# Performance work log

Hardware: AMD Instinct MI355X
Metric: run time of the kernel (lower is better)

Reference implementation:

```python
import jax, jax.numpy as jnp
import numpy as np

B, N, J, P = 64, 2048, 32, 64   # instances, ops per instance, jobs, ops per job (N = J*P)
D, H = 128, 128                 # out_size_ope, hidden_size_ope
NEG_SLOPE = 0.2


def _kaiming(key, fan_in, fan_out):
    return jax.random.normal(key, (fan_in, fan_out), jnp.float32) * np.sqrt(2.0 / fan_in)


def _mlp(x, W1, b1, W2, b2):
    # nn.Sequential(Linear, ELU, Linear)
    return jax.nn.elu(x @ W1 + b1) @ W2 + b2


def setup_inputs() -> dict:
    key = jax.random.key(0)
    ks = jax.random.split(key, 4)
    features = jax.random.normal(ks[0], (B, N, D), jnp.float32)
    job_starts = jnp.arange(J, dtype=jnp.int32) * P                      # first op of each job block
    offsets = jax.random.randint(ks[1], (B, J), 0, P)                    # current position within block
    ope_step_batch = job_starts[None, :] + offsets                       # [B, J], step_j in [start_j, end_j]
    end_ope_biases_batch = jnp.broadcast_to(job_starts + (P - 1), (B, J))
    opes_appertain_batch = jnp.broadcast_to(jnp.repeat(jnp.arange(J, dtype=jnp.int32), P)[None, :], (B, N))
    batch_idxes = jnp.arange(B, dtype=jnp.int32)
    inp = {
        'features': features,
        'discount_r': jnp.float32(0.9),
        'ope_step_batch': ope_step_batch,
        'end_ope_biases_batch': end_ope_biases_batch,
        'opes_appertain_batch': opes_appertain_batch,
        'batch_idxes': batch_idxes,
    }
    for i, nm in enumerate(['fw', 'zj', 'pr']):
        k1, k2 = jax.random.split(jax.random.fold_in(ks[2], i))
        inp[nm + '_W1'] = _kaiming(k1, D, H)
        inp[nm + '_b1'] = jnp.zeros((H,), jnp.float32)
        inp[nm + '_W2'] = _kaiming(k2, H, D)
        inp[nm + '_b2'] = jnp.zeros((D,), jnp.float32)
    return inp


def reference(features, discount_r,
              fw_W1, fw_b1, fw_W2, fw_b2,
              zj_W1, zj_b1, zj_W2, zj_b2,
              pr_W1, pr_b1, pr_W2, pr_b2,
              ope_step_batch, end_ope_biases_batch, opes_appertain_batch, batch_idxes):
    # opes_appertain_batch is accepted but unused, exactly like the torch forward.
    f32 = features.dtype
    steps = ope_step_batch[batch_idxes]        # [B, J]
    ends = end_ope_biases_batch[batch_idxes]   # [B, J]
    i = jnp.arange(N)

    # --- per-job descending update loop, vectorized ---
    # op i is updated iff step_j < i <= end_j for its job j; descending order in the
    # original means feat[i-1] is still the ORIGINAL value, so updates are independent.
    memb = (i[None, None, :] > steps[:, :, None]) & (i[None, None, :] <= ends[:, :, None])  # [B,J,N]
    updated = jnp.any(memb, axis=1)                                                         # [B,N]
    step_of = jnp.sum(jnp.where(memb, steps[:, :, None], 0), axis=1)                        # [B,N]
    rpow = discount_r ** (i[None, :] - step_of).astype(f32)                                 # r^(i - step)
    feat_prev = jnp.concatenate([jnp.zeros_like(features[:, :1]), features[:, :-1]], axis=1)
    # aggregate(MEAN): agg_f_w(feat_pre) + agg_f_w(feat_sub * r)
    cand = _mlp(features, fw_W1, fw_b1, fw_W2, fw_b2) + \
           _mlp(feat_prev * rpow[..., None], fw_W1, fw_b1, fw_W2, fw_b2)
    feat1 = jnp.where(updated[..., None], cand, features)

    # --- collect feat at each valid job's current step (step positions are never updated) ---
    collected = jax.vmap(lambda f, s: f[s])(features, steps)   # [B, J, D]
    valid = steps <= ends                                      # [B, J]
    n = jnp.sum(valid, axis=1).astype(f32)                     # [B]
    S = jnp.sum(jnp.where(valid[..., None], collected, 0.0), axis=1)  # [B, D]
    # aggregate_dif: new[j] = agg_z_j((old[j] + r * sum_{k!=j} old[k]) / n)
    mixed = (collected + discount_r * (S[:, None, :] - collected)) / n[:, None, None]
    z = _mlp(mixed, zj_W1, zj_b1, zj_W2, zj_b2)                # [B, J, D]

    # faithful replication of feat_opt[b][save_index[k]] = features_all[k]
    # (writes at op positions equal to JOB indices 0..J-1, for valid jobs)
    head = jnp.where(valid[..., None], z, feat1[:, :J, :])
    feat2 = feat1.at[:, :J, :].set(head)

    out = jax.nn.leaky_relu(_mlp(feat2, pr_W1, pr_b1, pr_W2, pr_b2), NEG_SLOPE)
    return out
```

## Files before the change

### kernel.cpp

```cpp
#include <hip/hip_runtime.h>

#define B_ 64
#define N_ 2048
#define J_ 32
#define D_ 128
#define NEG_SLOPE_ 0.2f

typedef __attribute__((ext_vector_type(4))) float f32x4;
typedef __attribute__((ext_vector_type(8))) __bf16 bf16x8;
typedef __attribute__((ext_vector_type(4))) __bf16 bf16x4;

#define ACT_NONE 0
#define ACT_ELU 1
#define ACT_LEAKY 2

template<int ACT>
__device__ __forceinline__ float apply_act(float v) {
    if constexpr (ACT == ACT_ELU)        return v > 0.f ? v : __expf(v) - 1.f;
    else if constexpr (ACT == ACT_LEAKY) return v >= 0.f ? v : NEG_SLOPE_ * v;
    else return v;
}

__device__ __forceinline__ bf16x8 frag_ld(const __bf16* src, int row, int kc) {
    return *(const bf16x8*)&src[row * D_ + ((kc ^ (row & 7)) << 3)];
}

__device__ __forceinline__ void load_wregs2(const __bf16* __restrict__ wmat,
                                            int wst, int ln, int lq, bf16x8 wr_[4][2]) {
#pragma unroll
    for (int ks = 0; ks < 4; ++ks)
#pragma unroll
        for (int mt = 0; mt < 2; ++mt)
            wr_[ks][mt] = frag_ld(wmat, wst * 32 + mt * 16 + ln, ks * 4 + lq);
}

__device__ __forceinline__ void gemmS(const __bf16* xb, const bf16x8 wr_[4][2],
                                      int ln, int lq, f32x4 acc[2][4]) {
    const f32x4 z = {0.f, 0.f, 0.f, 0.f};
#pragma unroll
    for (int mt = 0; mt < 2; ++mt)
#pragma unroll
        for (int nt = 0; nt < 4; ++nt) acc[mt][nt] = z;
#pragma unroll
    for (int ks = 0; ks < 4; ++ks) {
        const int kc = ks * 4 + lq;
        bf16x8 b[4];
#pragma unroll
        for (int nt = 0; nt < 4; ++nt) b[nt] = frag_ld(xb, nt * 16 + ln, kc);
#pragma unroll
        for (int mt = 0; mt < 2; ++mt)
#pragma unroll
            for (int nt = 0; nt < 4; ++nt)
                acc[mt][nt] = __builtin_amdgcn_mfma_f32_16x16x32_bf16(wr_[ks][mt], b[nt], acc[mt][nt], 0, 0, 0);
    }
}

template<bool INIT>
__device__ __forceinline__ void gemmS32(const __bf16* xb, const bf16x8 wr_[4][2],
                                        int ln, int lq, f32x4 acc[2][2]) {
    if constexpr (INIT) {
        const f32x4 z = {0.f, 0.f, 0.f, 0.f};
        acc[0][0] = z; acc[0][1] = z; acc[1][0] = z; acc[1][1] = z;
    }
#pragma unroll
    for (int ks = 0; ks < 4; ++ks) {
        const int kc = ks * 4 + lq;
        const bf16x8 b0 = frag_ld(xb, ln, kc);
        const bf16x8 b1 = frag_ld(xb, 16 + ln, kc);
#pragma unroll
        for (int mt = 0; mt < 2; ++mt) {
            acc[mt][0] = __builtin_amdgcn_mfma_f32_16x16x32_bf16(wr_[ks][mt], b0, acc[mt][0], 0, 0, 0);
            acc[mt][1] = __builtin_amdgcn_mfma_f32_16x16x32_bf16(wr_[ks][mt], b1, acc[mt][1], 0, 0, 0);
        }
    }
}

template<int ACT>
__device__ __forceinline__ void epiS_lds(const f32x4 acc[2][4], __bf16* dst,
                                         const float* __restrict__ bias,
                                         int wst, int ln, int lq) {
#pragma unroll
    for (int mt = 0; mt < 2; ++mt) {
        const int cb = wst * 32 + mt * 16 + lq * 4;
        const f32x4 bv = *(const f32x4*)&bias[cb];
#pragma unroll
        for (int nt = 0; nt < 4; ++nt) {
            const int jr = nt * 16 + ln;
            bf16x4 o;
#pragma unroll
            for (int r = 0; r < 4; ++r)
                o[r] = (__bf16)apply_act<ACT>(acc[mt][nt][r] + bv[r]);
            *(bf16x4*)&dst[jr * D_ + (((cb >> 3) ^ (jr & 7)) << 3) + (cb & 7)] = o;
        }
    }
}

template<int ACT>
__device__ __forceinline__ void epiS32_lds(const f32x4 acc[2][2], __bf16* dst, int rowoff,
                                           const float* __restrict__ bias,
                                           int wst, int ln, int lq) {
#pragma unroll
    for (int mt = 0; mt < 2; ++mt) {
        const int cb = wst * 32 + mt * 16 + lq * 4;
        const f32x4 bv = *(const f32x4*)&bias[cb];
#pragma unroll
        for (int nt = 0; nt < 2; ++nt) {
            const int jr = rowoff + nt * 16 + ln;
            bf16x4 o;
#pragma unroll
            for (int r = 0; r < 4; ++r)
                o[r] = (__bf16)apply_act<ACT>(acc[mt][nt][r] + bv[r]);
            *(bf16x4*)&dst[jr * D_ + (((cb >> 3) ^ (jr & 7)) << 3) + (cb & 7)] = o;
        }
    }
}

__global__ __launch_bounds__(256) void k_prep(
    const float* __restrict__ w0, const float* __restrict__ w1,
    const float* __restrict__ w2, const float* __restrict__ w3,
    const float* __restrict__ w4, const float* __restrict__ w5,
    __bf16* __restrict__ wdst,
    const float* __restrict__ F, const int* __restrict__ STEP,
    const int* __restrict__ ENDB, const int* __restrict__ BIDX,
    float* __restrict__ Sbuf, int* __restrict__ nvalid) {
    const int t = threadIdx.x;
    if (blockIdx.x < 6) {
        const float* src;
        switch (blockIdx.x) {
            case 0: src = w0; break; case 1: src = w1; break; case 2: src = w2; break;
            case 3: src = w3; break; case 4: src = w4; break; default: src = w5; break;
        }
        __bf16* d = wdst + (size_t)blockIdx.x * D_ * D_;
        for (int id = t; id < D_ * 16; id += 256) {
            const int n = id >> 4, ch = id & 15;
            bf16x8 u;
#pragma unroll
            for (int j = 0; j < 8; ++j) u[j] = (__bf16)src[(ch * 8 + j) * D_ + n];
            *(bf16x8*)&d[n * D_ + ((ch ^ (n & 7)) << 3)] = u;
        }
        return;
    }
    const int b = blockIdx.x - 6;
    __shared__ int steps_s[J_];
    __shared__ int valid_s[J_];
    __shared__ int nv;
    const int bi = BIDX[b];
    if (t == 0) nv = 0;
    __syncthreads();
    if (t < J_) {
        const int s = STEP[bi * J_ + t];
        const int e = ENDB[bi * J_ + t];
        steps_s[t] = s;
        const int v = (s <= e) ? 1 : 0;
        valid_s[t] = v;
        if (v) atomicAdd(&nv, 1);
    }
    __syncthreads();
    if (t < D_) {
        float acc = 0.f;
        for (int j = 0; j < J_; ++j)
            if (valid_s[j]) acc += F[((size_t)b * N_ + steps_s[j]) * D_ + t];
        Sbuf[b * D_ + t] = acc;
    }
    if (t == 0) nvalid[b] = nv;
}

__global__ __launch_bounds__(256, 4) void k_fused(
    const float* __restrict__ F, const float* __restrict__ rp_,
    const __bf16* __restrict__ wsW,
    const float* __restrict__ fb1, const float* __restrict__ fb2,
    const float* __restrict__ zb1, const float* __restrict__ zb2,
    const float* __restrict__ pb1, const float* __restrict__ pb2,
    const int* __restrict__ STEP, const int* __restrict__ ENDB,
    const int* __restrict__ BIDX, const float* __restrict__ Sbuf,
    const int* __restrict__ nvalid, float* __restrict__ out) {
    __shared__ __bf16 xs[64 * D_];
    __shared__ __bf16 hs[64 * D_];

    const int t = threadIdx.x;
    const int lane = t & 63, wst = t >> 6;
    const int ln = lane & 15, lq = lane >> 4;
    const int bid = blockIdx.x;
    const int b = bid >> 6, ti = bid & 63;
    const int r0 = ti * 32;
    const int bi = BIDX[b];
    const int jb = ti >> 1;
    const int s_j = STEP[bi * J_ + jb];
    const int e_j = ENDB[bi * J_ + jb];
    const float r = *rp_;
    const float l2r = __log2f(r);
    const int lo = (s_j + 1 > r0) ? s_j + 1 : r0;
    const int hi = (e_j < r0 + 31) ? e_j : r0 + 31;
    const bool has_upd = lo <= hi;
    const bool head_tile = (ti == 0);

    const float* Fb = F + (size_t)b * N_ * D_;
    const int nstage = (has_upd ? 64 : 32) * 16;
    for (int id = t; id < nstage; id += 256) {
        const int rr = id >> 4, ch = id & 15;
        bf16x8 u;
        if (rr < 32) {
            const float* fr = Fb + (size_t)(r0 + rr) * D_ + ch * 8;
            const float4 f0 = *(const float4*)fr, f1 = *(const float4*)(fr + 4);
            u[0] = (__bf16)f0.x; u[1] = (__bf16)f0.y; u[2] = (__bf16)f0.z; u[3] = (__bf16)f0.w;
            u[4] = (__bf16)f1.x; u[5] = (__bf16)f1.y; u[6] = (__bf16)f1.z; u[7] = (__bf16)f1.w;
        } else {
            const int i = r0 + rr - 32;
            const bool upd = (i > s_j) && (i <= e_j);
            if (upd) {
                const float sc = exp2f((float)(i - s_j) * l2r);
                const float* fr = Fb + (size_t)(i - 1) * D_ + ch * 8;
                const float4 f0 = *(const float4*)fr, f1 = *(const float4*)(fr + 4);
                u[0] = (__bf16)(f0.x * sc); u[1] = (__bf16)(f0.y * sc);
                u[2] = (__bf16)(f0.z * sc); u[3] = (__bf16)(f0.w * sc);
                u[4] = (__bf16)(f1.x * sc); u[5] = (__bf16)(f1.y * sc);
                u[6] = (__bf16)(f1.z * sc); u[7] = (__bf16)(f1.w * sc);
            } else {
#pragma unroll
                for (int j = 0; j < 8; ++j) u[j] = (__bf16)0.f;
            }
        }
        *(bf16x8*)&xs[rr * D_ + ((ch ^ (rr & 7)) << 3)] = u;
    }
    __syncthreads();

    if (has_upd) {
        {
            bf16x8 w1r[4][2];
            load_wregs2(wsW, wst, ln, lq, w1r);
            f32x4 acc[2][4];
            gemmS(xs, w1r, ln, lq, acc);
            epiS_lds<ACT_ELU>(acc, hs, fb1, wst, ln, lq);
        }
        __syncthreads();
        {
            bf16x8 w2r[4][2];
            load_wregs2(wsW + 16384, wst, ln, lq, w2r);
            f32x4 a2[2][2];
            gemmS32<true>(hs, w2r, ln, lq, a2);
            gemmS32<false>(hs + 32 * D_, w2r, ln, lq, a2);
#pragma unroll
            for (int nt = 0; nt < 2; ++nt) {
                const int row = nt * 16 + ln;
                const int i = r0 + row;
                if (!((i > s_j) && (i <= e_j))) continue;
#pragma unroll
                for (int mt = 0; mt < 2; ++mt) {
                    const int cb = wst * 32 + mt * 16 + lq * 4;
                    const f32x4 bv = *(const f32x4*)&fb2[cb];
                    bf16x4 o;
#pragma unroll
                    for (int rr2 = 0; rr2 < 4; ++rr2)
                        o[rr2] = (__bf16)(a2[mt][nt][rr2] + 2.f * bv[rr2]);
                    *(bf16x4*)&xs[row * D_ + (((cb >> 3) ^ (row & 7)) << 3) + (cb & 7)] = o;
                }
            }
        }
        __syncthreads();
    }

    if (head_tile) {
        const float n_ = (float)nvalid[b];
        const float inv = (n_ > 0.f) ? 1.f / n_ : 0.f;
        for (int id = t; id < 32 * 16; id += 256) {
            const int row = id >> 4, ch = id & 15;
            const int sr = STEP[bi * J_ + row];
            const float* cr = Fb + (size_t)sr * D_ + ch * 8;
            const float4 c0 = *(const float4*)cr, c1 = *(const float4*)(cr + 4);
            const float4 s0 = *(const float4*)(Sbuf + b * D_ + ch * 8);
            const float4 s1 = *(const float4*)(Sbuf + b * D_ + ch * 8 + 4);
            bf16x8 u;
            u[0] = (__bf16)((c0.x + r * (s0.x - c0.x)) * inv);
            u[1] = (__bf16)((c0.y + r * (s0.y - c0.y)) * inv);
            u[2] = (__bf16)((c0.z + r * (s0.z - c0.z)) * inv);
            u[3] = (__bf16)((c0.w + r * (s0.w - c0.w)) * inv);
            u[4] = (__bf16)((c1.x + r * (s1.x - c1.x)) * inv);
            u[5] = (__bf16)((c1.y + r * (s1.y - c1.y)) * inv);
            u[6] = (__bf16)((c1.z + r * (s1.z - c1.z)) * inv);
            u[7] = (__bf16)((c1.w + r * (s1.w - c1.w)) * inv);
            *(bf16x8*)&hs[row * D_ + ((ch ^ (row & 7)) << 3)] = u;
        }
        __syncthreads();
        {
            bf16x8 wza[4][2];
            load_wregs2(wsW + 4 * 16384, wst, ln, lq, wza);
            f32x4 az[2][2];
            gemmS32<true>(hs, wza, ln, lq, az);
            epiS32_lds<ACT_ELU>(az, hs, 32, zb1, wst, ln, lq);
        }
        __syncthreads();
        {
            bf16x8 wzb[4][2];
            load_wregs2(wsW + 5 * 16384, wst, ln, lq, wzb);
            f32x4 az[2][2];
            gemmS32<true>(hs + 32 * D_, wzb, ln, lq, az);
#pragma unroll
            for (int nt = 0; nt < 2; ++nt) {
                const int row = nt * 16 + ln;
                const int sr = STEP[bi * J_ + row];
                const int er = ENDB[bi * J_ + row];
                if (sr > er) continue;
#pragma unroll
                for (int mt = 0; mt < 2; ++mt) {
                    const int cb = wst * 32 + mt * 16 + lq * 4;
                    const f32x4 bv = *(const f32x4*)&zb2[cb];
                    bf16x4 o;
#pragma unroll
                    for (int rr2 = 0; rr2 < 4; ++rr2)
                        o[rr2] = (__bf16)(az[mt][nt][rr2] + bv[rr2]);
                    *(bf16x4*)&xs[row * D_ + (((cb >> 3) ^ (row & 7)) << 3) + (cb & 7)] = o;
                }
            }
        }
        __syncthreads();
    }

    {
        bf16x8 p1r[4][2];
        load_wregs2(wsW + 2 * 16384, wst, ln, lq, p1r);
        f32x4 ap[2][2];
        gemmS32<true>(xs, p1r, ln, lq, ap);
        epiS32_lds<ACT_ELU>(ap, hs, 0, pb1, wst, ln, lq);
    }
    __syncthreads();
    {
        bf16x8 p2r[4][2];
        load_wregs2(wsW + 3 * 16384, wst, ln, lq, p2r);
        f32x4 ap[2][2];
        gemmS32<true>(hs, p2r, ln, lq, ap);
        float* outb = out + ((size_t)b * N_ + r0) * D_;
#pragma unroll
        for (int mt = 0; mt < 2; ++mt) {
            const int cb = wst * 32 + mt * 16 + lq * 4;
            const f32x4 bv = *(const f32x4*)&pb2[cb];
#pragma unroll
            for (int nt = 0; nt < 2; ++nt) {
                const int jr = nt * 16 + ln;
                f32x4 o;
#pragma unroll
                for (int rr2 = 0; rr2 < 4; ++rr2)
                    o[rr2] = apply_act<ACT_LEAKY>(ap[mt][nt][rr2] + bv[rr2]);
                *(f32x4*)&outb[(size_t)jr * D_ + cb] = o;
            }
        }
    }
}

extern "C" void kernel_launch(void* const* d_in, const int* in_sizes, int n_in,
                              void* d_out, int out_size, void* d_ws, size_t ws_size,
                              hipStream_t stream) {
    const float* F    = (const float*)d_in[0];
    const float* rp   = (const float*)d_in[1];
    const int*  STEP  = (const int*)d_in[2];
    const int*  ENDB  = (const int*)d_in[3];
    const int*  BIDX  = (const int*)d_in[5];
    const float* fwW1 = (const float*)d_in[6];
    const float* fwb1 = (const float*)d_in[7];
    const float* fwW2 = (const float*)d_in[8];
    const float* fwb2 = (const float*)d_in[9];
    const float* zjW1 = (const float*)d_in[10];
    const float* zjb1 = (const float*)d_in[11];
    const float* zjW2 = (const float*)d_in[12];
    const float* zjb2 = (const float*)d_in[13];
    const float* prW1 = (const float*)d_in[14];
    const float* prb1 = (const float*)d_in[15];
    const float* prW2 = (const float*)d_in[16];
    const float* prb2 = (const float*)d_in[17];
    float* out = (float*)d_out;

    char* ws = (char*)d_ws;
    __bf16* wsW = (__bf16*)ws;
    float* Sbuf = (float*)(ws + 393216);
    int* nvalid = (int*)(ws + 425984);

    hipLaunchKernelGGL(k_prep, dim3(70), dim3(256), 0, stream,
                       fwW1, fwW2, prW1, prW2, zjW1, zjW2, wsW,
                       F, STEP, ENDB, BIDX, Sbuf, nvalid);
    hipLaunchKernelGGL(k_fused, dim3(B_ * 64), dim3(256), 0, stream,
                       F, rp, wsW, fwb1, fwb2, zjb1, zjb2, prb1, prb2,
                       STEP, ENDB, BIDX, Sbuf, nvalid, out);
}
```

Before: 67.74 us.

## Prefetch weight fragments early and restructure staging loads per thread

Staging of the feature tile is rewritten so each thread issues all its global loads (two direct rows plus two shifted, scaled rows) up front, with no loop or branches. The LDS weight fragments for the next GEMM stage are loaded into registers before the preceding epilogue or barrier, overlapping LDS latency with compute. Barriers are reordered so non-update, non-head tiles skip some synchronisation. This raises register pressure because two weight fragment sets are live at once, which could lower occupancy.

```diff
diff --git a/kernel.cpp b/kernel.cpp
--- a/kernel.cpp
+++ b/kernel.cpp
@@ -32,6 +32,16 @@
 #pragma unroll
         for (int mt = 0; mt < 2; ++mt)
             wr_[ks][mt] = frag_ld(wmat, wst * 32 + mt * 16 + ln, ks * 4 + lq);
+}
+
+__device__ __forceinline__ void st_row(__bf16* dst, int row, int ch,
+                                       float4 f0, float4 f1, float s) {
+    bf16x8 u;
+    u[0] = (__bf16)(f0.x * s); u[1] = (__bf16)(f0.y * s);
+    u[2] = (__bf16)(f0.z * s); u[3] = (__bf16)(f0.w * s);
+    u[4] = (__bf16)(f1.x * s); u[5] = (__bf16)(f1.y * s);
+    u[6] = (__bf16)(f1.z * s); u[7] = (__bf16)(f1.w * s);
+    *(bf16x8*)&dst[row * D_ + ((ch ^ (row & 7)) << 3)] = u;
 }
 
 __device__ __forceinline__ void gemmS(const __bf16* xb, const bf16x8 wr_[4][2],
@@ -195,74 +205,71 @@
     const bool head_tile = (ti == 0);
 
     const float* Fb = F + (size_t)b * N_ * D_;
-    const int nstage = (has_upd ? 64 : 32) * 16;
-    for (int id = t; id < nstage; id += 256) {
-        const int rr = id >> 4, ch = id & 15;
-        bf16x8 u;
-        if (rr < 32) {
-            const float* fr = Fb + (size_t)(r0 + rr) * D_ + ch * 8;
-            const float4 f0 = *(const float4*)fr, f1 = *(const float4*)(fr + 4);
-            u[0] = (__bf16)f0.x; u[1] = (__bf16)f0.y; u[2] = (__bf16)f0.z; u[3] = (__bf16)f0.w;
-            u[4] = (__bf16)f1.x; u[5] = (__bf16)f1.y; u[6] = (__bf16)f1.z; u[7] = (__bf16)f1.w;
-        } else {
-            const int i = r0 + rr - 32;
-            const bool upd = (i > s_j) && (i <= e_j);
-            if (upd) {
-                const float sc = exp2f((float)(i - s_j) * l2r);
-                const float* fr = Fb + (size_t)(i - 1) * D_ + ch * 8;
-                const float4 f0 = *(const float4*)fr, f1 = *(const float4*)(fr + 4);
-                u[0] = (__bf16)(f0.x * sc); u[1] = (__bf16)(f0.y * sc);
-                u[2] = (__bf16)(f0.z * sc); u[3] = (__bf16)(f0.w * sc);
-                u[4] = (__bf16)(f1.x * sc); u[5] = (__bf16)(f1.y * sc);
-                u[6] = (__bf16)(f1.z * sc); u[7] = (__bf16)(f1.w * sc);
-            } else {
-#pragma unroll
-                for (int j = 0; j < 8; ++j) u[j] = (__bf16)0.f;
+    const int rr_ = t >> 4;
+    const int ch_ = t & 15;
+    const int rA = r0 + rr_, rB = rA + 16;
+    const float* qA = Fb + (size_t)rA * D_ + ch_ * 8;
+    const float* qB = Fb + (size_t)rB * D_ + ch_ * 8;
+    const float4 xa0 = *(const float4*)qA, xa1 = *(const float4*)(qA + 4);
+    const float4 xb0 = *(const float4*)qB, xb1 = *(const float4*)(qB + 4);
+    float4 ya0, ya1, yb0, yb1;
+    float scA = 0.f, scB = 0.f;
+    if (has_upd) {
+        const bool uA = (rA > s_j) && (rA <= e_j);
+        const bool uB = (rB > s_j) && (rB <= e_j);
+        scA = uA ? exp2f((float)(rA - s_j) * l2r) : 0.f;
+        scB = uB ? exp2f((float)(rB - s_j) * l2r) : 0.f;
+        const float* uqA = Fb + (size_t)(uA ? rA - 1 : rA) * D_ + ch_ * 8;
+        const float* uqB = Fb + (size_t)(uB ? rB - 1 : rB) * D_ + ch_ * 8;
+        ya0 = *(const float4*)uqA; ya1 = *(const float4*)(uqA + 4);
+        yb0 = *(const float4*)uqB; yb1 = *(const float4*)(uqB + 4);
+    }
+    bf16x8 wA[4][2];
+    load_wregs2(has_upd ? wsW : wsW + 2 * 16384, wst, ln, lq, wA);
+
+    st_row(xs, rr_, ch_, xa0, xa1, 1.f);
+    st_row(xs, rr_ + 16, ch_, xb0, xb1, 1.f);
+    if (has_upd) {
+        st_row(xs, rr_ + 32, ch_, ya0, ya1, scA);
+        st_row(xs, rr_ + 48, ch_, yb0, yb1, scB);
+    }
+    __syncthreads();
+
+    if (has_upd) {
+        f32x4 acc[2][4];
+        gemmS(xs, wA, ln, lq, acc);
+        bf16x8 wB[4][2];
+        load_wregs2(wsW + 16384, wst, ln, lq, wB);
+        epiS_lds<ACT_ELU>(acc, hs, fb1, wst, ln, lq);
+        __syncthreads();
+        f32x4 a2[2][2];
+        gemmS32<true>(hs, wB, ln, lq, a2);
+        gemmS32<false>(hs + 32 * D_, wB, ln, lq, a2);
+#pragma unroll
+        for (int nt = 0; nt < 2; ++nt) {
+            const int row = nt * 16 + ln;
+            const int i = r0 + row;
+            if (!((i > s_j) && (i <= e_j))) continue;
+#pragma unroll
+            for (int mt = 0; mt < 2; ++mt) {
+                const int cb = wst * 32 + mt * 16 + lq * 4;
+                const f32x4 bv = *(const f32x4*)&fb2[cb];
+                bf16x4 o;
+#pragma unroll
+                for (int rr2 = 0; rr2 < 4; ++rr2)
+                    o[rr2] = (__bf16)(a2[mt][nt][rr2] + 2.f * bv[rr2]);
+                *(bf16x4*)&xs[row * D_ + (((cb >> 3) ^ (row & 7)) << 3) + (cb & 7)] = o;
             }
         }
-        *(bf16x8*)&xs[rr * D_ + ((ch ^ (rr & 7)) << 3)] = u;
-    }
-    __syncthreads();
-
-    if (has_upd) {
-        {
-            bf16x8 w1r[4][2];
-            load_wregs2(wsW, wst, ln, lq, w1r);
-            f32x4 acc[2][4];
-            gemmS(xs, w1r, ln, lq, acc);
-            epiS_lds<ACT_ELU>(acc, hs, fb1, wst, ln, lq);
-        }
+    }
+
+    if (head_tile) {
         __syncthreads();
-        {
-            bf16x8 w2r[4][2];
-            load_wregs2(wsW + 16384, wst, ln, lq, w2r);
-            f32x4 a2[2][2];
-            gemmS32<true>(hs, w2r, ln, lq, a2);
-            gemmS32<false>(hs + 32 * D_, w2r, ln, lq, a2);
-#pragma unroll
-            for (int nt = 0; nt < 2; ++nt) {
-                const int row = nt * 16 + ln;
-                const int i = r0 + row;
-                if (!((i > s_j) && (i <= e_j))) continue;
-#pragma unroll
-                for (int mt = 0; mt < 2; ++mt) {
-                    const int cb = wst * 32 + mt * 16 + lq * 4;
-                    const f32x4 bv = *(const f32x4*)&fb2[cb];
-                    bf16x4 o;
-#pragma unroll
-                    for (int rr2 = 0; rr2 < 4; ++rr2)
-                        o[rr2] = (__bf16)(a2[mt][nt][rr2] + 2.f * bv[rr2]);
-                    *(bf16x4*)&xs[row * D_ + (((cb >> 3) ^ (row & 7)) << 3) + (cb & 7)] = o;
-                }
-            }
-        }
-        __syncthreads();
-    }
-
-    if (head_tile) {
         const float n_ = (float)nvalid[b];
         const float inv = (n_ > 0.f) ? 1.f / n_ : 0.f;
-        for (int id = t; id < 32 * 16; id += 256) {
+#pragma unroll
+        for (int it = 0; it < 2; ++it) {
+            const int id = t + it * 256;
             const int row = id >> 4, ch = id & 15;
             const int sr = STEP[bi * J_ + row];
             const float* cr = Fb + (size_t)sr * D_ + ch * 8;
@@ -312,36 +319,33 @@
                 }
             }
         }
-        __syncthreads();
-    }
-
-    {
-        bf16x8 p1r[4][2];
-        load_wregs2(wsW + 2 * 16384, wst, ln, lq, p1r);
-        f32x4 ap[2][2];
-        gemmS32<true>(xs, p1r, ln, lq, ap);
-        epiS32_lds<ACT_ELU>(ap, hs, 0, pb1, wst, ln, lq);
-    }
-    __syncthreads();
-    {
-        bf16x8 p2r[4][2];
-        load_wregs2(wsW + 3 * 16384, wst, ln, lq, p2r);
-        f32x4 ap[2][2];
-        gemmS32<true>(hs, p2r, ln, lq, ap);
-        float* outb = out + ((size_t)b * N_ + r0) * D_;
-#pragma unroll
-        for (int mt = 0; mt < 2; ++mt) {
-            const int cb = wst * 32 + mt * 16 + lq * 4;
-            const f32x4 bv = *(const f32x4*)&pb2[cb];
-#pragma unroll
-            for (int nt = 0; nt < 2; ++nt) {
-                const int jr = nt * 16 + ln;
-                f32x4 o;
-#pragma unroll
-                for (int rr2 = 0; rr2 < 4; ++rr2)
-                    o[rr2] = apply_act<ACT_LEAKY>(ap[mt][nt][rr2] + bv[rr2]);
-                *(f32x4*)&outb[(size_t)jr * D_ + cb] = o;
-            }
+    }
+
+    if (has_upd || head_tile)
+        load_wregs2(wsW + 2 * 16384, wst, ln, lq, wA);
+    __syncthreads();
+
+    f32x4 ap[2][2];
+    gemmS32<true>(xs, wA, ln, lq, ap);
+    bf16x8 wB2[4][2];
+    load_wregs2(wsW + 3 * 16384, wst, ln, lq, wB2);
+    epiS32_lds<ACT_ELU>(ap, hs, 0, pb1, wst, ln, lq);
+    __syncthreads();
+
+    gemmS32<true>(hs, wB2, ln, lq, ap);
+    float* outb = out + ((size_t)b * N_ + r0) * D_;
+#pragma unroll
+    for (int mt = 0; mt < 2; ++mt) {
+        const int cb = wst * 32 + mt * 16 + lq * 4;
+        const f32x4 bv = *(const f32x4*)&pb2[cb];
+#pragma unroll
+        for (int nt = 0; nt < 2; ++nt) {
+            const int jr = nt * 16 + ln;
+            f32x4 o;
+#pragma unroll
+            for (int rr2 = 0; rr2 < 4; ++rr2)
+                o[rr2] = apply_act<ACT_LEAKY>(ap[mt][nt][rr2] + bv[rr2]);
+            *(f32x4*)&outb[(size_t)jr * D_ + cb] = o;
         }
     }
 }
```

Result: faster. 64.69 us (-4.5%).
